# Kernel optimization log

Measured on AMD Instinct MI355X. Metric: run time of the kernel, lower is better.

## Reference

```python
import jax, jax.numpy as jnp
import numpy as np

HUGE = 1e9  # stand-in for ops.HUGE_INT


def setup_inputs() -> dict:
    key = jax.random.key(0)
    ks = jax.random.split(key, 8)
    B, Q, K = 8, 128, 256
    Dq = Dk = Dv = H = 512
    query = jax.random.normal(ks[0], (B, Q, Dq), dtype=jnp.float32)
    k_ = jax.random.normal(ks[1], (B, K, Dk), dtype=jnp.float32)
    value = jax.random.normal(ks[2], (B, K, Dv), dtype=jnp.float32)
    mask = jax.random.randint(ks[3], (B, K), 0, 2, dtype=jnp.int32)
    # FFN params: linear1 (Dq+Dk -> H, bias), linear2 (H -> 1, no bias)
    W1 = jax.random.normal(ks[4], (Dq + Dk, H), dtype=jnp.float32) * 0.05
    b1 = jax.random.normal(ks[5], (H,), dtype=jnp.float32) * 0.05
    w2 = jax.random.normal(ks[6], (H, 1), dtype=jnp.float32) * 0.05
    return {"query": query, "key": k_, "value": value, "mask": mask,
            "W1": W1, "b1": b1, "w2": w2}


def reference(query, key, value, mask, W1, b1, w2):
    # Additive (FFN) attention. Original tiles query/key into [B, Q*K, Dq+Dk]
    # and applies linear1; concat@W1 is separable, so we project q and k
    # separately and broadcast-add (same math, no tiled concat tensor).
    Dq = query.shape[-1]
    Wq, Wk = W1[:Dq], W1[Dq:]
    q_proj = jnp.einsum('bqd,dh->bqh', query, Wq)   # [B,Q,H]
    k_proj = jnp.einsum('bkd,dh->bkh', key, Wk)     # [B,K,H]
    hidden = jnp.tanh(q_proj[:, :, None, :] + k_proj[:, None, :, :] + b1)  # [B,Q,K,H]
    scores = jnp.einsum('bqkh,h->bqk', hidden, w2[:, 0])  # [B,Q,K]
    # padding mask fill BEFORE scaling, matching the original op order
    scores = jnp.where(mask[:, None, :] != 0, -HUGE, scores)
    scores = scores / jnp.sqrt(jnp.float32(key.shape[-1]))
    attn_weights = jax.nn.softmax(scores, axis=-1)
    attn_vec = jnp.einsum('bqk,bkv->bqv', attn_weights, value)  # dropout=0 at eval
    return attn_vec, attn_weights
```

## Files before the change

kernel.cpp:

```cpp
#include <hip/hip_runtime.h>
#include <hip/hip_bf16.h>

#define B_ 8
#define Q_ 128
#define K_ 256
#define D_ 512
#define TWOLOG2E 2.8853900817779268f
#define SCALE 0.044194173824159216f
#define L2E 1.4426950408889634f
#define MASKVAL (-44194173.824159216f)

typedef __attribute__((ext_vector_type(8))) short frag8;
typedef __attribute__((ext_vector_type(4))) float f32x4;

__device__ __forceinline__ float fexp2(float x) {
  float r;
  asm("v_exp_f32 %0, %1" : "=v"(r) : "v"(x));
  return r;
}
__device__ __forceinline__ float frcp(float x) {
  float r;
  asm("v_rcp_f32 %0, %1" : "=v"(r) : "v"(x));
  return r;
}
__device__ __forceinline__ unsigned f2bf_u(float x) {
  unsigned u = __float_as_uint(x);
  return (u + 0x7FFFu + ((u >> 16) & 1u)) >> 16;
}
__device__ __forceinline__ unsigned short f2bf(float x) {
  return (unsigned short)f2bf_u(x);
}
__device__ __forceinline__ unsigned packbf(float lo, float hi) {
  return f2bf_u(lo) | (f2bf_u(hi) << 16);
}

__global__ __launch_bounds__(256) void gemm_kernel(
    const float* __restrict__ query, const float* __restrict__ key,
    const float* __restrict__ W1, const float* __restrict__ b1,
    float* __restrict__ qp, float* __restrict__ kpbT) {
  __shared__ short As[32 * 64];
  __shared__ short Bs[64 * 72];
  const int t = threadIdx.x;
  const int m0 = blockIdx.y * 32;
  const int n0 = blockIdx.x * 64;
  const bool is_k = (m0 >= B_ * Q_);
  const float* X = is_k ? key : query;
  const int xrow0 = is_k ? (m0 - B_ * Q_) : m0;
  const float* Wb = W1 + (is_k ? (size_t)D_ * D_ : 0);

  const int am = t >> 3;
  const int ac = t & 7;
  const float* gA = X + (size_t)(xrow0 + am) * D_ + ac * 8;
  short* aw = As + am * 64 + ((ac ^ (am & 7)) * 8);

  const int prow = t >> 4;
  const int n4 = (t & 15) * 4;
  const float* gB = Wb + n0 + n4;

  const int l = t & 63;
  const int w = t >> 6;
  const int lr = l & 15;
  const int kg = l >> 4;
  const int key8 = lr & 7;
  int aoff[2][2], boff[2];
#pragma unroll
  for (int kk = 0; kk < 2; ++kk) {
    const int cposA = ((kg + kk * 4) ^ key8) * 8;
#pragma unroll
    for (int mt = 0; mt < 2; ++mt) aoff[mt][kk] = (mt * 16 + lr) * 64 + cposA;
    boff[kk] = (w * 16 + lr) * 72 + (kg + kk * 4) * 8;
  }

  f32x4 acc[2];
  acc[0] = (f32x4){0.f, 0.f, 0.f, 0.f};
  acc[1] = (f32x4){0.f, 0.f, 0.f, 0.f};

  for (int k0 = 0; k0 < D_; k0 += 64) {
    float4 a0 = *(const float4*)(gA + k0);
    float4 a1 = *(const float4*)(gA + k0 + 4);
    float4 w00 = *(const float4*)(gB + (size_t)(k0 + 2 * prow) * D_);
    float4 w01 = *(const float4*)(gB + (size_t)(k0 + 2 * prow + 1) * D_);
    float4 w10 = *(const float4*)(gB + (size_t)(k0 + 2 * prow + 32) * D_);
    float4 w11 = *(const float4*)(gB + (size_t)(k0 + 2 * prow + 33) * D_);
    __syncthreads();
    {
      union { frag8 f; unsigned short u[8]; } av;
      av.u[0] = f2bf(a0.x); av.u[1] = f2bf(a0.y); av.u[2] = f2bf(a0.z); av.u[3] = f2bf(a0.w);
      av.u[4] = f2bf(a1.x); av.u[5] = f2bf(a1.y); av.u[6] = f2bf(a1.z); av.u[7] = f2bf(a1.w);
      *(frag8*)aw = av.f;
    }
    {
      float lo0[4] = {w00.x, w00.y, w00.z, w00.w};
      float hi0[4] = {w01.x, w01.y, w01.z, w01.w};
      float lo1[4] = {w10.x, w10.y, w10.z, w10.w};
      float hi1[4] = {w11.x, w11.y, w11.z, w11.w};
#pragma unroll
      for (int j = 0; j < 4; ++j) {
        *(unsigned*)(Bs + (n4 + j) * 72 + 2 * prow) = packbf(lo0[j], hi0[j]);
        *(unsigned*)(Bs + (n4 + j) * 72 + 2 * (prow + 16)) = packbf(lo1[j], hi1[j]);
      }
    }
    __syncthreads();
#pragma unroll
    for (int kk = 0; kk < 2; ++kk) {
      frag8 bf = *(const frag8*)(Bs + boff[kk]);
#pragma unroll
      for (int mt = 0; mt < 2; ++mt) {
        frag8 af = *(const frag8*)(As + aoff[mt][kk]);
        acc[mt] = __builtin_amdgcn_mfma_f32_16x16x32_bf16(af, bf, acc[mt], 0, 0, 0);
      }
    }
  }

  const int col = n0 + w * 16 + lr;
  if (is_k) {
    const float bc = b1[col];
#pragma unroll
    for (int mt = 0; mt < 2; ++mt) {
      const int krow = m0 - B_ * Q_ + mt * 16 + kg * 4;
      const int bb = krow >> 8;
      const int kk0 = krow & 255;
      float4 v;
      v.x = fexp2((acc[mt][0] + bc) * TWOLOG2E);
      v.y = fexp2((acc[mt][1] + bc) * TWOLOG2E);
      v.z = fexp2((acc[mt][2] + bc) * TWOLOG2E);
      v.w = fexp2((acc[mt][3] + bc) * TWOLOG2E);
      *(float4*)&kpbT[((size_t)bb * D_ + col) * K_ + kk0] = v;
    }
  } else {
#pragma unroll
    for (int mt = 0; mt < 2; ++mt) {
#pragma unroll
      for (int i = 0; i < 4; ++i) {
        const int row = m0 + mt * 16 + kg * 4 + i;
        qp[(size_t)row * D_ + col] = fexp2(acc[mt][i] * TWOLOG2E);
      }
    }
  }
}

__global__ __launch_bounds__(1024) void attn_kernel(
    const float* __restrict__ qp, const float* __restrict__ kpbT,
    const float* __restrict__ value, const int* __restrict__ mask,
    const float* __restrict__ w2,
    float* __restrict__ out_vec, float* __restrict__ out_w) {
  __shared__ float smem_p[16 * 512];
  __shared__ float pw[4 * 256];
  const int b = blockIdx.y;
  const int q0 = blockIdx.x * 4;
  const int t = threadIdx.x;
  const int lane = t & 63;
  const int w = __builtin_amdgcn_readfirstlane(t >> 6);
  const int kc = w & 1;
  const int hq = w >> 1;
  const int h0 = hq * 64;

  {
    const float* pk = kpbT + ((size_t)b * D_ + h0) * K_ + kc * 128 + 2 * lane;
    const float* q_0 = qp + (size_t)(b * Q_ + q0 + 0) * D_ + h0;
    const float* q_1 = qp + (size_t)(b * Q_ + q0 + 1) * D_ + h0;
    const float* q_2 = qp + (size_t)(b * Q_ + q0 + 2) * D_ + h0;
    const float* q_3 = qp + (size_t)(b * Q_ + q0 + 3) * D_ + h0;
    const float* w2h = w2 + h0;

    float2 a0 = {0.f, 0.f}, a1 = {0.f, 0.f}, a2 = {0.f, 0.f}, a3 = {0.f, 0.f};
    for (int h = 0; h < 64; h += 8) {
      float2 kv[8];
#pragma unroll
      for (int j = 0; j < 8; ++j) kv[j] = *(const float2*)&pk[(size_t)(h + j) * K_];
      float4 e0a = *(const float4*)(q_0 + h), e0b = *(const float4*)(q_0 + h + 4);
      float4 e1a = *(const float4*)(q_1 + h), e1b = *(const float4*)(q_1 + h + 4);
      float4 e2a = *(const float4*)(q_2 + h), e2b = *(const float4*)(q_2 + h + 4);
      float4 e3a = *(const float4*)(q_3 + h), e3b = *(const float4*)(q_3 + h + 4);
      float4 wa = *(const float4*)(w2h + h), wb = *(const float4*)(w2h + h + 4);
      float E0[8] = {e0a.x, e0a.y, e0a.z, e0a.w, e0b.x, e0b.y, e0b.z, e0b.w};
      float E1[8] = {e1a.x, e1a.y, e1a.z, e1a.w, e1b.x, e1b.y, e1b.z, e1b.w};
      float E2[8] = {e2a.x, e2a.y, e2a.z, e2a.w, e2b.x, e2b.y, e2b.z, e2b.w};
      float E3[8] = {e3a.x, e3a.y, e3a.z, e3a.w, e3b.x, e3b.y, e3b.z, e3b.w};
      float WV[8] = {wa.x, wa.y, wa.z, wa.w, wb.x, wb.y, wb.z, wb.w};
#pragma unroll
      for (int j = 0; j < 8; ++j) {
        a0.x = fmaf(WV[j], frcp(fmaf(E0[j], kv[j].x, 1.f)), a0.x);
        a0.y = fmaf(WV[j], frcp(fmaf(E0[j], kv[j].y, 1.f)), a0.y);
        a1.x = fmaf(WV[j], frcp(fmaf(E1[j], kv[j].x, 1.f)), a1.x);
        a1.y = fmaf(WV[j], frcp(fmaf(E1[j], kv[j].y, 1.f)), a1.y);
        a2.x = fmaf(WV[j], frcp(fmaf(E2[j], kv[j].x, 1.f)), a2.x);
        a2.y = fmaf(WV[j], frcp(fmaf(E2[j], kv[j].y, 1.f)), a2.y);
        a3.x = fmaf(WV[j], frcp(fmaf(E3[j], kv[j].x, 1.f)), a3.x);
        a3.y = fmaf(WV[j], frcp(fmaf(E3[j], kv[j].y, 1.f)), a3.y);
      }
    }
    *(float2*)&smem_p[w * 512 + 0 * 128 + 2 * lane] = a0;
    *(float2*)&smem_p[w * 512 + 1 * 128 + 2 * lane] = a1;
    *(float2*)&smem_p[w * 512 + 2 * 128 + 2 * lane] = a2;
    *(float2*)&smem_p[w * 512 + 3 * 128 + 2 * lane] = a3;
  }
  __syncthreads();

  if (w < 4) {
    const int q = w;
    float sw = 0.f;
#pragma unroll
    for (int m = 0; m < 8; ++m) sw += w2[lane + 64 * m];
#pragma unroll
    for (int off = 32; off; off >>= 1) sw += __shfl_xor(sw, off);

    float s[4];
#pragma unroll
    for (int r = 0; r < 4; ++r) {
      const int kcc = r >> 1;
      const int off = (r & 1) * 64 + lane;
      float p = 0.f;
#pragma unroll
      for (int hh = 0; hh < 8; ++hh)
        p += smem_p[(hh * 2 + kcc) * 512 + q * 128 + off];
      const int mk = mask[b * K_ + r * 64 + lane];
      s[r] = mk ? MASKVAL : fmaf(-2.f, p, sw) * SCALE;
    }
    float mx = fmaxf(fmaxf(s[0], s[1]), fmaxf(s[2], s[3]));
#pragma unroll
    for (int off = 32; off; off >>= 1) mx = fmaxf(mx, __shfl_xor(mx, off));
    float e[4], sum = 0.f;
#pragma unroll
    for (int r = 0; r < 4; ++r) {
      e[r] = fexp2((s[r] - mx) * L2E);
      sum += e[r];
    }
#pragma unroll
    for (int off = 32; off; off >>= 1) sum += __shfl_xor(sum, off);
    const float inv = frcp(sum);
    float* ow = out_w + (size_t)(b * Q_ + q0 + q) * K_;
#pragma unroll
    for (int r = 0; r < 4; ++r) {
      const float p = e[r] * inv;
      pw[q * 256 + r * 64 + lane] = p;
      ow[r * 64 + lane] = p;
    }
  }
  __syncthreads();

  const int col = t & 511;
  const int qq = t >> 9;
  float o0 = 0.f, o1 = 0.f;
  const float* vb = value + (size_t)b * K_ * D_;
  for (int k = 0; k < K_; k += 4) {
    const float4 p0 = *(const float4*)&pw[(qq * 2 + 0) * 256 + k];
    const float4 p1 = *(const float4*)&pw[(qq * 2 + 1) * 256 + k];
    const float v0 = vb[(size_t)(k + 0) * D_ + col];
    const float v1 = vb[(size_t)(k + 1) * D_ + col];
    const float v2 = vb[(size_t)(k + 2) * D_ + col];
    const float v3 = vb[(size_t)(k + 3) * D_ + col];
    o0 = fmaf(p0.x, v0, fmaf(p0.y, v1, fmaf(p0.z, v2, fmaf(p0.w, v3, o0))));
    o1 = fmaf(p1.x, v0, fmaf(p1.y, v1, fmaf(p1.z, v2, fmaf(p1.w, v3, o1))));
  }
  out_vec[(size_t)(b * Q_ + q0 + qq * 2 + 0) * D_ + col] = o0;
  out_vec[(size_t)(b * Q_ + q0 + qq * 2 + 1) * D_ + col] = o1;
}

extern "C" void kernel_launch(void* const* d_in, const int* in_sizes, int n_in,
                              void* d_out, int out_size, void* d_ws, size_t ws_size,
                              hipStream_t stream) {
  const float* query = (const float*)d_in[0];
  const float* key   = (const float*)d_in[1];
  const float* value = (const float*)d_in[2];
  const int*   mask  = (const int*)d_in[3];
  const float* W1    = (const float*)d_in[4];
  const float* b1    = (const float*)d_in[5];
  const float* w2    = (const float*)d_in[6];

  float* out_vec = (float*)d_out;
  float* out_w   = out_vec + (size_t)B_ * Q_ * D_;

  float* qp   = (float*)d_ws;
  float* kpbT = qp + (size_t)B_ * Q_ * D_;

  gemm_kernel<<<dim3(8, 96), 256, 0, stream>>>(query, key, W1, b1, qp, kpbT);
  attn_kernel<<<dim3(Q_ / 4, B_), 1024, 0, stream>>>(qp, kpbT, value, mask, w2,
                                                     out_vec, out_w);
}
```

Before: 111.6 us.

## Split attention into score and PV kernels with larger query tiles

Splits the fused attention kernel into a score/softmax kernel and a separate PV kernel. The PV kernel tiles 32 queries by 64 columns per block, so each value element is reused across more queries. This reduces redundant reads of the value matrix. In exchange it adds an extra kernel launch and a round trip of the attention weights through global memory.

```diff
diff --git a/kernel.cpp b/kernel.cpp
--- a/kernel.cpp
+++ b/kernel.cpp
@@ -139,13 +139,11 @@
   }
 }
 
-__global__ __launch_bounds__(1024) void attn_kernel(
+__global__ __launch_bounds__(1024) void score_kernel(
     const float* __restrict__ qp, const float* __restrict__ kpbT,
-    const float* __restrict__ value, const int* __restrict__ mask,
-    const float* __restrict__ w2,
-    float* __restrict__ out_vec, float* __restrict__ out_w) {
+    const int* __restrict__ mask, const float* __restrict__ w2,
+    float* __restrict__ out_w) {
   __shared__ float smem_p[16 * 512];
-  __shared__ float pw[4 * 256];
   const int b = blockIdx.y;
   const int q0 = blockIdx.x * 4;
   const int t = threadIdx.x;
@@ -231,30 +229,39 @@
     const float inv = frcp(sum);
     float* ow = out_w + (size_t)(b * Q_ + q0 + q) * K_;
 #pragma unroll
-    for (int r = 0; r < 4; ++r) {
-      const float p = e[r] * inv;
-      pw[q * 256 + r * 64 + lane] = p;
-      ow[r * 64 + lane] = p;
-    }
-  }
-  __syncthreads();
-
-  const int col = t & 511;
-  const int qq = t >> 9;
+    for (int r = 0; r < 4; ++r) ow[r * 64 + lane] = e[r] * inv;
+  }
+}
+
+__global__ __launch_bounds__(1024) void pv_kernel(
+    const float* __restrict__ out_w, const float* __restrict__ value,
+    float* __restrict__ out_vec) {
+  const int b = blockIdx.y;
+  const int qt = blockIdx.x >> 3;
+  const int ct = blockIdx.x & 7;
+  const int t = threadIdx.x;
+  const int lane = t & 63;
+  const int w = __builtin_amdgcn_readfirstlane(t >> 6);
+  const int col = ct * 64 + lane;
+  const int q0 = qt * 32 + w * 2;
+
+  const float* pw0 = out_w + (size_t)(b * Q_ + q0) * K_;
+  const float* pw1 = pw0 + K_;
+  const float* vb = value + (size_t)b * K_ * D_ + col;
+
   float o0 = 0.f, o1 = 0.f;
-  const float* vb = value + (size_t)b * K_ * D_;
   for (int k = 0; k < K_; k += 4) {
-    const float4 p0 = *(const float4*)&pw[(qq * 2 + 0) * 256 + k];
-    const float4 p1 = *(const float4*)&pw[(qq * 2 + 1) * 256 + k];
-    const float v0 = vb[(size_t)(k + 0) * D_ + col];
-    const float v1 = vb[(size_t)(k + 1) * D_ + col];
-    const float v2 = vb[(size_t)(k + 2) * D_ + col];
-    const float v3 = vb[(size_t)(k + 3) * D_ + col];
+    const float4 p0 = *(const float4*)&pw0[k];
+    const float4 p1 = *(const float4*)&pw1[k];
+    const float v0 = vb[(size_t)(k + 0) * D_];
+    const float v1 = vb[(size_t)(k + 1) * D_];
+    const float v2 = vb[(size_t)(k + 2) * D_];
+    const float v3 = vb[(size_t)(k + 3) * D_];
     o0 = fmaf(p0.x, v0, fmaf(p0.y, v1, fmaf(p0.z, v2, fmaf(p0.w, v3, o0))));
     o1 = fmaf(p1.x, v0, fmaf(p1.y, v1, fmaf(p1.z, v2, fmaf(p1.w, v3, o1))));
   }
-  out_vec[(size_t)(b * Q_ + q0 + qq * 2 + 0) * D_ + col] = o0;
-  out_vec[(size_t)(b * Q_ + q0 + qq * 2 + 1) * D_ + col] = o1;
+  out_vec[(size_t)(b * Q_ + q0) * D_ + col] = o0;
+  out_vec[(size_t)(b * Q_ + q0 + 1) * D_ + col] = o1;
 }
 
 extern "C" void kernel_launch(void* const* d_in, const int* in_sizes, int n_in,
@@ -275,6 +282,6 @@
   float* kpbT = qp + (size_t)B_ * Q_ * D_;
 
   gemm_kernel<<<dim3(8, 96), 256, 0, stream>>>(query, key, W1, b1, qp, kpbT);
-  attn_kernel<<<dim3(Q_ / 4, B_), 1024, 0, stream>>>(qp, kpbT, value, mask, w2,
-                                                     out_vec, out_w);
-}
+  score_kernel<<<dim3(Q_ / 4, B_), 1024, 0, stream>>>(qp, kpbT, mask, w2, out_w);
+  pv_kernel<<<dim3(32, B_), 1024, 0, stream>>>(out_w, value, out_vec);
+}
```

Result: slower. 113.9 us (+2.0%).

## Compact unmasked keys and skip score computation for masked positions

Applied to the files above, without the earlier changes.

The projection kernel now writes the transformed key projections in a compacted order that holds only unmasked keys, using a ballot and prefix count over the mask. The attention kernel builds an index list of unmasked keys, and when at most 128 are present it splits the hidden dimension across all 16 waves over half the key range, halving the tanh/rcp work. Scores are scattered back to their original positions, with masked slots prefilled by the mask value. This adds extra synchronisation and shared-memory scatter, and the saving depends on how many keys the input masks out.

```diff
diff --git a/kernel.cpp b/kernel.cpp
--- a/kernel.cpp
+++ b/kernel.cpp
@@ -37,9 +37,12 @@
 __global__ __launch_bounds__(256) void gemm_kernel(
     const float* __restrict__ query, const float* __restrict__ key,
     const float* __restrict__ W1, const float* __restrict__ b1,
+    const int* __restrict__ mask,
     float* __restrict__ qp, float* __restrict__ kpbT) {
   __shared__ short As[32 * 64];
   __shared__ short Bs[64 * 72];
+  __shared__ int posm[K_];
+  __shared__ int cnt4[4];
   const int t = threadIdx.x;
   const int m0 = blockIdx.y * 32;
   const int n0 = blockIdx.x * 64;
@@ -114,18 +117,38 @@
 
   const int col = n0 + w * 16 + lr;
   if (is_k) {
+    const int bb = (m0 - B_ * Q_) >> 8;
+    {
+      const bool um = (mask[bb * K_ + t] == 0);
+      const unsigned long long bal = __ballot(um);
+      const int pic = (int)__popcll(bal & ((1ull << l) - 1ull));
+      posm[t] = um ? pic : -1;
+      if (l == 0) cnt4[w] = (int)__popcll(bal);
+    }
+    __syncthreads();
+    if (posm[t] >= 0) {
+      int base = 0;
+#pragma unroll
+      for (int j = 0; j < 3; ++j)
+        if (j < w) base += cnt4[j];
+      posm[t] += base;
+    }
+    __syncthreads();
+
     const float bc = b1[col];
 #pragma unroll
     for (int mt = 0; mt < 2; ++mt) {
-      const int krow = m0 - B_ * Q_ + mt * 16 + kg * 4;
-      const int bb = krow >> 8;
-      const int kk0 = krow & 255;
-      float4 v;
-      v.x = fexp2((acc[mt][0] + bc) * TWOLOG2E);
-      v.y = fexp2((acc[mt][1] + bc) * TWOLOG2E);
-      v.z = fexp2((acc[mt][2] + bc) * TWOLOG2E);
-      v.w = fexp2((acc[mt][3] + bc) * TWOLOG2E);
-      *(float4*)&kpbT[((size_t)bb * D_ + col) * K_ + kk0] = v;
+      const int kk0 = (m0 - B_ * Q_ + mt * 16 + kg * 4) & 255;
+      float vv[4];
+      vv[0] = fexp2((acc[mt][0] + bc) * TWOLOG2E);
+      vv[1] = fexp2((acc[mt][1] + bc) * TWOLOG2E);
+      vv[2] = fexp2((acc[mt][2] + bc) * TWOLOG2E);
+      vv[3] = fexp2((acc[mt][3] + bc) * TWOLOG2E);
+#pragma unroll
+      for (int i = 0; i < 4; ++i) {
+        const int p = posm[kk0 + i];
+        if (p >= 0) kpbT[((size_t)bb * D_ + col) * K_ + p] = vv[i];
+      }
     }
   } else {
 #pragma unroll
@@ -146,14 +169,33 @@
     float* __restrict__ out_vec, float* __restrict__ out_w) {
   __shared__ float smem_p[16 * 512];
   __shared__ float pw[4 * 256];
+  __shared__ int idxl[K_];
+  __shared__ int sM;
   const int b = blockIdx.y;
   const int q0 = blockIdx.x * 4;
   const int t = threadIdx.x;
   const int lane = t & 63;
   const int w = __builtin_amdgcn_readfirstlane(t >> 6);
-  const int kc = w & 1;
-  const int hq = w >> 1;
-  const int h0 = hq * 64;
+
+  if (w == 0) {
+    int base = 0;
+#pragma unroll
+    for (int c = 0; c < 4; ++c) {
+      const int k = c * 64 + lane;
+      const int mk = mask[b * K_ + k];
+      const unsigned long long bal = __ballot(mk == 0);
+      const int pos = (int)__popcll(bal & ((1ull << lane) - 1ull));
+      if (mk == 0) idxl[base + pos] = k;
+      base += (int)__popcll(bal);
+    }
+    if (lane == 0) sM = base;
+  }
+  __syncthreads();
+  const int M = sM;
+  const bool big = (M > 128);
+  const int kc = big ? (w & 1) : 0;
+  const int h0 = big ? (w >> 1) * 64 : w * 32;
+  const int hlen = big ? 64 : 32;
 
   {
     const float* pk = kpbT + ((size_t)b * D_ + h0) * K_ + kc * 128 + 2 * lane;
@@ -164,7 +206,7 @@
     const float* w2h = w2 + h0;
 
     float2 a0 = {0.f, 0.f}, a1 = {0.f, 0.f}, a2 = {0.f, 0.f}, a3 = {0.f, 0.f};
-    for (int h = 0; h < 64; h += 8) {
+    for (int h = 0; h < hlen; h += 8) {
       float2 kv[8];
 #pragma unroll
       for (int j = 0; j < 8; ++j) kv[j] = *(const float2*)&pk[(size_t)(h + j) * K_];
@@ -205,25 +247,39 @@
 #pragma unroll
     for (int off = 32; off; off >>= 1) sw += __shfl_xor(sw, off);
 
-    float s[4];
+#pragma unroll
+    for (int r = 0; r < 4; ++r) pw[q * 256 + r * 64 + lane] = MASKVAL;
 #pragma unroll
     for (int r = 0; r < 4; ++r) {
-      const int kcc = r >> 1;
-      const int off = (r & 1) * 64 + lane;
+      const int slot = r * 64 + lane;
       float p = 0.f;
-#pragma unroll
-      for (int hh = 0; hh < 8; ++hh)
-        p += smem_p[(hh * 2 + kcc) * 512 + q * 128 + off];
-      const int mk = mask[b * K_ + r * 64 + lane];
-      s[r] = mk ? MASKVAL : fmaf(-2.f, p, sw) * SCALE;
-    }
-    float mx = fmaxf(fmaxf(s[0], s[1]), fmaxf(s[2], s[3]));
+      if (big) {
+        const int kcc = r >> 1;
+        const int off = (r & 1) * 64 + lane;
+#pragma unroll
+        for (int i = 0; i < 8; ++i)
+          p += smem_p[(2 * i + kcc) * 512 + q * 128 + off];
+      } else {
+        if (r < 2) {
+#pragma unroll
+          for (int ww = 0; ww < 16; ++ww)
+            p += smem_p[ww * 512 + q * 128 + slot];
+        }
+      }
+      const bool valid = (slot < M) && (big || r < 2);
+      if (valid) pw[q * 256 + idxl[slot]] = fmaf(-2.f, p, sw) * SCALE;
+    }
+
+    float sv[4];
+#pragma unroll
+    for (int r = 0; r < 4; ++r) sv[r] = pw[q * 256 + r * 64 + lane];
+    float mx = fmaxf(fmaxf(sv[0], sv[1]), fmaxf(sv[2], sv[3]));
 #pragma unroll
     for (int off = 32; off; off >>= 1) mx = fmaxf(mx, __shfl_xor(mx, off));
     float e[4], sum = 0.f;
 #pragma unroll
     for (int r = 0; r < 4; ++r) {
-      e[r] = fexp2((s[r] - mx) * L2E);
+      e[r] = fexp2((sv[r] - mx) * L2E);
       sum += e[r];
     }
 #pragma unroll
@@ -274,7 +330,7 @@
   float* qp   = (float*)d_ws;
   float* kpbT = qp + (size_t)B_ * Q_ * D_;
 
-  gemm_kernel<<<dim3(8, 96), 256, 0, stream>>>(query, key, W1, b1, qp, kpbT);
+  gemm_kernel<<<dim3(8, 96), 256, 0, stream>>>(query, key, W1, b1, mask, qp, kpbT);
   attn_kernel<<<dim3(Q_ / 4, B_), 1024, 0, stream>>>(qp, kpbT, value, mask, w2,
                                                      out_vec, out_w);
 }
```

Result: no change. 113.1 us (+1.3%).

## Halve queries per attention block to double grid size and rework wave split

Applied to the files above, without the earlier changes.

Each attention block now handles 2 queries instead of 4, and each wave covers 32 hidden units across all 256 keys with float4 key loads instead of splitting keys in halves. The grid doubles so more blocks can be resident per CU, improving latency hiding for the reciprocal-heavy score loop. The cost is less reuse of key projections and value rows per block, so L2 traffic roughly doubles for those tensors. The launch-bounds hint is also raised.

```diff
diff --git a/kernel.cpp b/kernel.cpp
--- a/kernel.cpp
+++ b/kernel.cpp
@@ -139,65 +139,55 @@
   }
 }
 
-__global__ __launch_bounds__(1024) void attn_kernel(
+__global__ __launch_bounds__(1024, 8) void attn_kernel(
     const float* __restrict__ qp, const float* __restrict__ kpbT,
     const float* __restrict__ value, const int* __restrict__ mask,
     const float* __restrict__ w2,
     float* __restrict__ out_vec, float* __restrict__ out_w) {
   __shared__ float smem_p[16 * 512];
-  __shared__ float pw[4 * 256];
+  __shared__ float pw[2 * 256];
   const int b = blockIdx.y;
-  const int q0 = blockIdx.x * 4;
+  const int q0 = blockIdx.x * 2;
   const int t = threadIdx.x;
   const int lane = t & 63;
   const int w = __builtin_amdgcn_readfirstlane(t >> 6);
-  const int kc = w & 1;
-  const int hq = w >> 1;
-  const int h0 = hq * 64;
+  const int h0 = w * 32;
 
   {
-    const float* pk = kpbT + ((size_t)b * D_ + h0) * K_ + kc * 128 + 2 * lane;
+    const float* pk = kpbT + ((size_t)b * D_ + h0) * K_ + lane * 4;
     const float* q_0 = qp + (size_t)(b * Q_ + q0 + 0) * D_ + h0;
     const float* q_1 = qp + (size_t)(b * Q_ + q0 + 1) * D_ + h0;
-    const float* q_2 = qp + (size_t)(b * Q_ + q0 + 2) * D_ + h0;
-    const float* q_3 = qp + (size_t)(b * Q_ + q0 + 3) * D_ + h0;
     const float* w2h = w2 + h0;
 
-    float2 a0 = {0.f, 0.f}, a1 = {0.f, 0.f}, a2 = {0.f, 0.f}, a3 = {0.f, 0.f};
-    for (int h = 0; h < 64; h += 8) {
-      float2 kv[8];
-#pragma unroll
-      for (int j = 0; j < 8; ++j) kv[j] = *(const float2*)&pk[(size_t)(h + j) * K_];
-      float4 e0a = *(const float4*)(q_0 + h), e0b = *(const float4*)(q_0 + h + 4);
-      float4 e1a = *(const float4*)(q_1 + h), e1b = *(const float4*)(q_1 + h + 4);
-      float4 e2a = *(const float4*)(q_2 + h), e2b = *(const float4*)(q_2 + h + 4);
-      float4 e3a = *(const float4*)(q_3 + h), e3b = *(const float4*)(q_3 + h + 4);
-      float4 wa = *(const float4*)(w2h + h), wb = *(const float4*)(w2h + h + 4);
-      float E0[8] = {e0a.x, e0a.y, e0a.z, e0a.w, e0b.x, e0b.y, e0b.z, e0b.w};
-      float E1[8] = {e1a.x, e1a.y, e1a.z, e1a.w, e1b.x, e1b.y, e1b.z, e1b.w};
-      float E2[8] = {e2a.x, e2a.y, e2a.z, e2a.w, e2b.x, e2b.y, e2b.z, e2b.w};
-      float E3[8] = {e3a.x, e3a.y, e3a.z, e3a.w, e3b.x, e3b.y, e3b.z, e3b.w};
-      float WV[8] = {wa.x, wa.y, wa.z, wa.w, wb.x, wb.y, wb.z, wb.w};
-#pragma unroll
-      for (int j = 0; j < 8; ++j) {
-        a0.x = fmaf(WV[j], frcp(fmaf(E0[j], kv[j].x, 1.f)), a0.x);
-        a0.y = fmaf(WV[j], frcp(fmaf(E0[j], kv[j].y, 1.f)), a0.y);
-        a1.x = fmaf(WV[j], frcp(fmaf(E1[j], kv[j].x, 1.f)), a1.x);
-        a1.y = fmaf(WV[j], frcp(fmaf(E1[j], kv[j].y, 1.f)), a1.y);
-        a2.x = fmaf(WV[j], frcp(fmaf(E2[j], kv[j].x, 1.f)), a2.x);
-        a2.y = fmaf(WV[j], frcp(fmaf(E2[j], kv[j].y, 1.f)), a2.y);
-        a3.x = fmaf(WV[j], frcp(fmaf(E3[j], kv[j].x, 1.f)), a3.x);
-        a3.y = fmaf(WV[j], frcp(fmaf(E3[j], kv[j].y, 1.f)), a3.y);
-      }
-    }
-    *(float2*)&smem_p[w * 512 + 0 * 128 + 2 * lane] = a0;
-    *(float2*)&smem_p[w * 512 + 1 * 128 + 2 * lane] = a1;
-    *(float2*)&smem_p[w * 512 + 2 * 128 + 2 * lane] = a2;
-    *(float2*)&smem_p[w * 512 + 3 * 128 + 2 * lane] = a3;
+    float4 a0 = {0.f, 0.f, 0.f, 0.f}, a1 = {0.f, 0.f, 0.f, 0.f};
+    for (int h = 0; h < 32; h += 4) {
+      float4 kv[4];
+#pragma unroll
+      for (int j = 0; j < 4; ++j) kv[j] = *(const float4*)&pk[(size_t)(h + j) * K_];
+      float4 E0 = *(const float4*)(q_0 + h);
+      float4 E1 = *(const float4*)(q_1 + h);
+      float4 WV = *(const float4*)(w2h + h);
+      float E0a[4] = {E0.x, E0.y, E0.z, E0.w};
+      float E1a[4] = {E1.x, E1.y, E1.z, E1.w};
+      float WVa[4] = {WV.x, WV.y, WV.z, WV.w};
+#pragma unroll
+      for (int j = 0; j < 4; ++j) {
+        a0.x = fmaf(WVa[j], frcp(fmaf(E0a[j], kv[j].x, 1.f)), a0.x);
+        a0.y = fmaf(WVa[j], frcp(fmaf(E0a[j], kv[j].y, 1.f)), a0.y);
+        a0.z = fmaf(WVa[j], frcp(fmaf(E0a[j], kv[j].z, 1.f)), a0.z);
+        a0.w = fmaf(WVa[j], frcp(fmaf(E0a[j], kv[j].w, 1.f)), a0.w);
+        a1.x = fmaf(WVa[j], frcp(fmaf(E1a[j], kv[j].x, 1.f)), a1.x);
+        a1.y = fmaf(WVa[j], frcp(fmaf(E1a[j], kv[j].y, 1.f)), a1.y);
+        a1.z = fmaf(WVa[j], frcp(fmaf(E1a[j], kv[j].z, 1.f)), a1.z);
+        a1.w = fmaf(WVa[j], frcp(fmaf(E1a[j], kv[j].w, 1.f)), a1.w);
+      }
+    }
+    *(float4*)&smem_p[w * 512 + 0 * 256 + lane * 4] = a0;
+    *(float4*)&smem_p[w * 512 + 1 * 256 + lane * 4] = a1;
   }
   __syncthreads();
 
-  if (w < 4) {
+  if (w < 2) {
     const int q = w;
     float sw = 0.f;
 #pragma unroll
@@ -208,13 +198,11 @@
     float s[4];
 #pragma unroll
     for (int r = 0; r < 4; ++r) {
-      const int kcc = r >> 1;
-      const int off = (r & 1) * 64 + lane;
+      const int k = r * 64 + lane;
       float p = 0.f;
 #pragma unroll
-      for (int hh = 0; hh < 8; ++hh)
-        p += smem_p[(hh * 2 + kcc) * 512 + q * 128 + off];
-      const int mk = mask[b * K_ + r * 64 + lane];
+      for (int ww = 0; ww < 16; ++ww) p += smem_p[ww * 512 + q * 256 + k];
+      const int mk = mask[b * K_ + k];
       s[r] = mk ? MASKVAL : fmaf(-2.f, p, sw) * SCALE;
     }
     float mx = fmaxf(fmaxf(s[0], s[1]), fmaxf(s[2], s[3]));
@@ -241,20 +229,18 @@
 
   const int col = t & 511;
   const int qq = t >> 9;
-  float o0 = 0.f, o1 = 0.f;
+  float o = 0.f;
   const float* vb = value + (size_t)b * K_ * D_;
+  const float* pwq = &pw[qq * 256];
   for (int k = 0; k < K_; k += 4) {
-    const float4 p0 = *(const float4*)&pw[(qq * 2 + 0) * 256 + k];
-    const float4 p1 = *(const float4*)&pw[(qq * 2 + 1) * 256 + k];
+    const float4 p = *(const float4*)&pwq[k];
     const float v0 = vb[(size_t)(k + 0) * D_ + col];
     const float v1 = vb[(size_t)(k + 1) * D_ + col];
     const float v2 = vb[(size_t)(k + 2) * D_ + col];
     const float v3 = vb[(size_t)(k + 3) * D_ + col];
-    o0 = fmaf(p0.x, v0, fmaf(p0.y, v1, fmaf(p0.z, v2, fmaf(p0.w, v3, o0))));
-    o1 = fmaf(p1.x, v0, fmaf(p1.y, v1, fmaf(p1.z, v2, fmaf(p1.w, v3, o1))));
-  }
-  out_vec[(size_t)(b * Q_ + q0 + qq * 2 + 0) * D_ + col] = o0;
-  out_vec[(size_t)(b * Q_ + q0 + qq * 2 + 1) * D_ + col] = o1;
+    o = fmaf(p.x, v0, fmaf(p.y, v1, fmaf(p.z, v2, fmaf(p.w, v3, o))));
+  }
+  out_vec[(size_t)(b * Q_ + q0 + qq) * D_ + col] = o;
 }
 
 extern "C" void kernel_launch(void* const* d_in, const int* in_sizes, int n_in,
@@ -275,6 +261,6 @@
   float* kpbT = qp + (size_t)B_ * Q_ * D_;
 
   gemm_kernel<<<dim3(8, 96), 256, 0, stream>>>(query, key, W1, b1, qp, kpbT);
-  attn_kernel<<<dim3(Q_ / 4, B_), 1024, 0, stream>>>(qp, kpbT, value, mask, w2,
+  attn_kernel<<<dim3(Q_ / 2, B_), 1024, 0, stream>>>(qp, kpbT, value, mask, w2,
                                                      out_vec, out_w);
 }
```

Result: slower. 196.0 us (+75.6%).
